# Performance work log

Hardware: AMD Instinct MI355X
Metric: run time of the kernel (lower is better)

## Reference

```python
import jax, jax.numpy as jnp
import numpy as np

HEADS, DIM_HEAD, DIM = 12, 64, 768
H = W = 32
N = H * W
B = 4


def _ln(x, g, b, eps=1e-5):
    mu = x.mean(-1, keepdims=True)
    var = ((x - mu) ** 2).mean(-1, keepdims=True)
    return (x - mu) / jnp.sqrt(var + eps) * g + b


def _get_epipolar(k, src_c2w, target_c2w, h=H, w=W):
    # Faithful port of Epipolar_Attention.get_epipolar, without the (hw*hw,3) repeat
    # materialization (uses broadcasting for the pairwise cross product instead).
    b = k.shape[0]
    Wf = h * 16.0 / 9.0
    k = k.astype(jnp.float32)
    k = k.at[:, 0, :].multiply(Wf).at[:, 1, :].multiply(float(h))
    k = k.at[:, 0, 2].set(h / 2.0).at[:, 1, 2].set(h / 2.0)
    ii, jj = jnp.meshgrid(jnp.arange(h), jnp.arange(w), indexing='ij')
    # after the torch column swap: (col, row, 1)
    coords = jnp.stack([jj.ravel(), ii.ravel(), jnp.ones(h * w, jnp.int32)], axis=1).astype(jnp.float32)  # [hw,3]
    k3 = k[:, :3, :3]
    src_r, src_t = src_c2w[:, :3, :3].astype(jnp.float32), src_c2w[:, :3, 3].astype(jnp.float32)
    tgt_r, tgt_t = target_c2w[:, :3, :3].astype(jnp.float32), target_c2w[:, :3, 3].astype(jnp.float32)
    tgt_rinv = jnp.linalg.inv(tgt_r)
    fx, fy = k3[:, 0, 0][:, None], k3[:, 1, 1][:, None]
    cx, cy = k3[:, 0, 2][:, None], k3[:, 1, 2][:, None]
    nc = jnp.stack([(coords[None, :, 0] - cx) / fx,
                    (coords[None, :, 1] - cy) / fy,
                    jnp.broadcast_to(coords[None, :, 2], (b, h * w))], axis=-1)  # [b,hw,3]
    p3w = jnp.einsum('bij,bnj->bni', src_r, nc) + src_t[:, None]
    p2 = jnp.einsum('bij,bnj->bni', tgt_rinv, p3w) - tgt_t[:, None]  # target_w2c_t = -target_c2w_t
    pij_un = jnp.einsum('bij,bnj->bni', k3, p2)                      # [b,hw,3]
    pij = pij_un / (pij_un[..., -1:] + 1e-6)
    o2 = jnp.einsum('bij,bj->bi', tgt_rinv, src_t) - tgt_t           # origin projected
    oij = jnp.einsum('bij,bj->bi', k3, o2)
    oij = oij / oij[..., -1:]
    oi_to_pi = pij - oij[:, None]                # [b,hw,3]
    oi_to_coord = coords[None] - oij[:, None]    # [b,hw,3]
    cr = jnp.cross(oi_to_pi[:, :, None, :], oi_to_coord[:, None, :, :])  # [b,hw,hw,3]
    area = jnp.sqrt((cr * cr).sum(-1))
    vlen = jnp.sqrt((oi_to_pi * oi_to_pi).sum(-1))[:, :, None]
    dist = area / vlen
    dw = 1.0 - jax.nn.sigmoid(50.0 * (dist - 0.5))
    row_max = dw.max(-1, keepdims=True)
    return jnp.where(row_max < 0.5, 1.0, dw)     # rows with max<0.5 are set to all-ones


def setup_inputs():
    key = jax.random.key(0)
    ks = jax.random.split(key, 16)
    s = 0.02
    x = jax.random.normal(ks[0], (B, N, DIM), jnp.float32)
    src_encode = jax.random.normal(ks[1], (B, N, DIM), jnp.float32)
    intrinsic = (jnp.zeros((B, 4, 4), jnp.float32)
                 .at[:, 0, 0].set(1.0).at[:, 1, 1].set(1.0)
                 .at[:, 0, 2].set(0.5).at[:, 1, 2].set(0.5)
                 .at[:, 2, 2].set(1.0).at[:, 3, 3].set(1.0))
    R = jnp.eye(3, dtype=jnp.float32) + 0.1 * jax.random.normal(ks[2], (2, B, 3, 3), jnp.float32)
    t = 0.5 * jax.random.normal(ks[3], (2, B, 3), jnp.float32)
    c2w = (jnp.zeros((2, B, 4, 4), jnp.float32)
           .at[:, :, :3, :3].set(R).at[:, :, :3, 3].set(t).at[:, :, 3, 3].set(1.0))
    hd = HEADS * DIM_HEAD
    w_ = lambda k_, shp: s * jax.random.normal(k_, shp, jnp.float32)
    return dict(
        x=x, src_encode=src_encode, intrinsic=intrinsic, c2w=c2w,
        lnq_g=jnp.ones(DIM), lnq_b=jnp.zeros(DIM), Wq=w_(ks[4], (DIM, hd)), bq=jnp.zeros(hd),
        lnk_g=jnp.ones(DIM), lnk_b=jnp.zeros(DIM), Wk=w_(ks[5], (DIM, hd)), bk=jnp.zeros(hd),
        lnv_g=jnp.ones(DIM), lnv_b=jnp.zeros(DIM), Wv=w_(ks[6], (DIM, hd)), bv=jnp.zeros(hd),
        Wp=w_(ks[7], (hd, DIM)), bp=jnp.zeros(DIM),
        pre_g=jnp.ones(DIM), pre_b=jnp.zeros(DIM),
        W1=w_(ks[8], (DIM, 2 * DIM)), b1=jnp.zeros(2 * DIM),
        W2=w_(ks[9], (2 * DIM, DIM)), b2=jnp.zeros(DIM),
        post_g=jnp.ones(DIM), post_b=jnp.zeros(DIM))


def reference(x, src_encode, intrinsic, c2w, lnq_g, lnq_b, Wq, bq, lnk_g, lnk_b, Wk, bk,
              lnv_g, lnv_b, Wv, bv, Wp, bp, pre_g, pre_b, W1, b1, W2, b2, post_g, post_b):
    b, n, _ = x.shape
    scale = DIM_HEAD ** -0.5
    split = lambda t_: t_.reshape(b, n, HEADS, DIM_HEAD).transpose(0, 2, 1, 3)  # [b,m,n,d]
    q = split(_ln(x, lnq_g, lnq_b) @ Wq + bq)
    k = split(_ln(src_encode, lnk_g, lnk_b) @ Wk + bk)
    v = split(_ln(src_encode, lnv_g, lnv_b) @ Wv + bv)
    scores = scale * jnp.einsum('bmqd,bmkd->bmqk', q, k)
    e1 = _get_epipolar(intrinsic, c2w[1], c2w[0])                    # do_epipolar
    e2 = jnp.swapaxes(_get_epipolar(intrinsic, c2w[0], c2w[1]), 1, 2)  # bidirectional (transposed)
    wmap = e1 * e2                                                   # [b,n,n], shared across heads
    att = jax.nn.softmax(scores * wmap[:, None], axis=-1)
    a = jnp.einsum('bmqk,bmkd->bmqd', att, v).transpose(0, 2, 1, 3).reshape(b, n, HEADS * DIM_HEAD)
    z = _ln(a @ Wp + bp, pre_g, pre_b)
    z = z + (jax.nn.gelu(z @ W1 + b1, approximate=False) @ W2 + b2)  # torch nn.GELU = exact erf
    z = _ln(z, post_g, post_b)
    wm_full = jnp.broadcast_to(wmap[:, None], (b, HEADS, n, n)).reshape(b * HEADS, n, n)
    return z, wm_full
```

## Files before the change

kernel.cpp:

```cpp
#include <hip/hip_runtime.h>
#include <hip/hip_bf16.h>

typedef unsigned short u16;
typedef __attribute__((ext_vector_type(4))) unsigned short u16x4;
typedef __attribute__((ext_vector_type(8))) unsigned short u16x8;
typedef __attribute__((ext_vector_type(8))) short s16x8;
typedef __attribute__((ext_vector_type(4))) float f32x4;

#define HEADS 12
#define NSEQ 1024
#define DIMM 768
#define DHEAD 64

__device__ __forceinline__ float b2f(u16 h) {
  union { unsigned u; float f; } v; v.u = ((unsigned)h) << 16; return v.f;
}
__device__ __forceinline__ u16 f2b(float f) {
  union { float f; unsigned u; } v; v.f = f;
  unsigned r = v.u + 0x7fffu + ((v.u >> 16) & 1u);
  return (u16)(r >> 16);
}
__device__ __forceinline__ void gl_lds16(const u16* g, u16* l) {
  __builtin_amdgcn_global_load_lds(
      (const __attribute__((address_space(1))) void*)g,
      (__attribute__((address_space(3))) void*)l, 16, 0, 0);
}

template<bool GELU, bool RESID>
__device__ __forceinline__ void gemm_body(
    const u16* __restrict__ A, const u16* __restrict__ BT,
    const float* __restrict__ bias, const u16* __restrict__ resid,
    const float* __restrict__ rg, const float* __restrict__ rb,
    u16* __restrict__ C, int K, int lda, int ldb, int ldc,
    int m0, int n0, u16* As, u16* Bs)
{
  const int tid = threadIdx.x;
  const int lane = tid & 63;
  const int wv = tid >> 6;
  const int wm0 = (wv >> 1) * 64;
  const int wn0 = (wv & 1) * 64;
  const int l15 = lane & 15;
  const int quad = lane >> 4;
  const int srow = lane >> 2;
  const int scol = (lane & 3) * 8;

  f32x4 acc[4][4];
  #pragma unroll
  for (int i = 0; i < 4; ++i)
    #pragma unroll
    for (int j = 0; j < 4; ++j)
      acc[i][j] = {0.f, 0.f, 0.f, 0.f};

  const u16* Ab = A + (long)(m0 + wv * 32 + srow) * lda + scol;
  const u16* Bb = BT + (long)(n0 + wv * 32 + srow) * ldb + scol;
  u16* AsW = As + (wv * 32) * 32;
  u16* BsW = Bs + (wv * 32) * 32;

  auto issue = [&](int buf, int kk) {
    #pragma unroll
    for (int t = 0; t < 2; ++t) {
      gl_lds16(Ab + kk + (long)t * 16 * lda, AsW + buf * 4096 + t * 16 * 32);
      gl_lds16(Bb + kk + (long)t * 16 * ldb, BsW + buf * 4096 + t * 16 * 32);
    }
  };

  const int NK = K >> 5;
  issue(0, 0);
  issue(1, 32);

  int cur = 0;
  for (int i = 0; i < NK; ++i) {
    if (i + 1 < NK) asm volatile("s_waitcnt vmcnt(4)" ::: "memory");
    else            asm volatile("s_waitcnt vmcnt(0)" ::: "memory");
    __builtin_amdgcn_s_barrier();
    __builtin_amdgcn_sched_barrier(0);
    if (i + 2 < NK) {
      int nb = cur + 2; if (nb >= 3) nb -= 3;
      issue(nb, (i + 2) * 32);
    }
    const u16* Ac = As + cur * 4096;
    const u16* Bc = Bs + cur * 4096;
    s16x8 af[4], bfr[4];
    #pragma unroll
    for (int i2 = 0; i2 < 4; ++i2)
      af[i2] = *(const s16x8*)&Ac[(wm0 + i2 * 16 + l15) * 32 + quad * 8];
    #pragma unroll
    for (int j = 0; j < 4; ++j)
      bfr[j] = *(const s16x8*)&Bc[(wn0 + j * 16 + l15) * 32 + quad * 8];
    #pragma unroll
    for (int i2 = 0; i2 < 4; ++i2)
      #pragma unroll
      for (int j = 0; j < 4; ++j)
        acc[i2][j] = __builtin_amdgcn_mfma_f32_16x16x32_bf16(af[i2], bfr[j], acc[i2][j], 0, 0, 0);
    ++cur; if (cur == 3) cur = 0;
  }

  #pragma unroll
  for (int i = 0; i < 4; ++i)
    #pragma unroll
    for (int j = 0; j < 4; ++j) {
      const int col = n0 + wn0 + j * 16 + l15;
      const float bvv = bias[col];
      #pragma unroll
      for (int v = 0; v < 4; ++v) {
        const int row = m0 + wm0 + i * 16 + quad * 4 + v;
        float val = acc[i][j][v] + bvv;
        if (GELU) val = 0.5f * val * (1.0f + erff(val * 0.70710678118654752440f));
        if (RESID) val += b2f(resid[(long)row * ldc + col]) * rg[col] + rb[col];
        C[(long)row * ldc + col] = f2b(val);
      }
    }
}

template<bool GELU, bool RESID>
__device__ __forceinline__ void gemm_body64(
    const u16* __restrict__ A, const u16* __restrict__ BT,
    const float* __restrict__ bias, const u16* __restrict__ resid,
    const float* __restrict__ rg, const float* __restrict__ rb,
    u16* __restrict__ C, int K, int lda, int ldb, int ldc,
    int m0, int n0, u16* As, u16* Bs)
{
  const int tid = threadIdx.x;
  const int lane = tid & 63;
  const int wv = tid >> 6;
  const int wm0 = wv * 32;
  const int l15 = lane & 15;
  const int quad = lane >> 4;
  const int srow = lane >> 2;
  const int scol = (lane & 3) * 8;

  f32x4 acc[2][4];
  #pragma unroll
  for (int i = 0; i < 2; ++i)
    #pragma unroll
    for (int j = 0; j < 4; ++j)
      acc[i][j] = {0.f, 0.f, 0.f, 0.f};

  const u16* Ab = A + (long)(m0 + wv * 32 + srow) * lda + scol;
  const u16* Bb = BT + (long)(n0 + wv * 16 + srow) * ldb + scol;
  u16* AsW = As + (wv * 32) * 32;
  u16* BsW = Bs + (wv * 16) * 32;

  auto issue = [&](int buf, int kk) {
    #pragma unroll
    for (int t = 0; t < 2; ++t)
      gl_lds16(Ab + kk + (long)t * 16 * lda, AsW + buf * 4096 + t * 16 * 32);
    gl_lds16(Bb + kk, BsW + buf * 2048);
  };

  const int NK = K >> 5;
  issue(0, 0);
  issue(1, 32);

  int cur = 0;
  for (int i = 0; i < NK; ++i) {
    if (i + 1 < NK) asm volatile("s_waitcnt vmcnt(3)" ::: "memory");
    else            asm volatile("s_waitcnt vmcnt(0)" ::: "memory");
    __builtin_amdgcn_s_barrier();
    __builtin_amdgcn_sched_barrier(0);
    if (i + 2 < NK) {
      int nb = cur + 2; if (nb >= 3) nb -= 3;
      issue(nb, (i + 2) * 32);
    }
    const u16* Ac = As + cur * 4096;
    const u16* Bc = Bs + cur * 2048;
    s16x8 af[2], bfr[4];
    #pragma unroll
    for (int i2 = 0; i2 < 2; ++i2)
      af[i2] = *(const s16x8*)&Ac[(wm0 + i2 * 16 + l15) * 32 + quad * 8];
    #pragma unroll
    for (int j = 0; j < 4; ++j)
      bfr[j] = *(const s16x8*)&Bc[(j * 16 + l15) * 32 + quad * 8];
    #pragma unroll
    for (int i2 = 0; i2 < 2; ++i2)
      #pragma unroll
      for (int j = 0; j < 4; ++j)
        acc[i2][j] = __builtin_amdgcn_mfma_f32_16x16x32_bf16(af[i2], bfr[j], acc[i2][j], 0, 0, 0);
    ++cur; if (cur == 3) cur = 0;
  }

  #pragma unroll
  for (int i = 0; i < 2; ++i)
    #pragma unroll
    for (int j = 0; j < 4; ++j) {
      const int col = n0 + j * 16 + l15;
      const float bvv = bias[col];
      #pragma unroll
      for (int v = 0; v < 4; ++v) {
        const int row = m0 + wm0 + i * 16 + quad * 4 + v;
        float val = acc[i][j][v] + bvv;
        if (GELU) val = 0.5f * val * (1.0f + erff(val * 0.70710678118654752440f));
        if (RESID) val += b2f(resid[(long)row * ldc + col]) * rg[col] + rb[col];
        C[(long)row * ldc + col] = f2b(val);
      }
    }
}

template<bool GELU, bool RESID>
__global__ __launch_bounds__(256)
void gemm_one(const u16* __restrict__ A, const u16* __restrict__ BT,
              const float* __restrict__ bias, const u16* __restrict__ resid,
              const float* __restrict__ rg, const float* __restrict__ rb,
              u16* __restrict__ C, int K, int lda, int ldb, int ldc)
{
  __shared__ u16 As[12288], Bs[6144];
  gemm_body64<GELU, RESID>(A, BT, bias, resid, rg, rb, C, K, lda, ldb, ldc,
                           blockIdx.x * 128, blockIdx.y * 64, As, Bs);
}

__global__ __launch_bounds__(256)
void gemm_qkv(const u16* __restrict__ nx, const u16* __restrict__ ns,
              const u16* __restrict__ qT, const u16* __restrict__ kvT,
              const float* __restrict__ bqf, const float* __restrict__ bkvf,
              u16* __restrict__ qb, u16* __restrict__ kvb)
{
  __shared__ u16 As[12288], Bs[12288];
  const int z = blockIdx.z;
  if (z == 0)
    gemm_body<false, false>(nx, qT, bqf, nullptr, nullptr, nullptr, qb,
                            768, 768, 768, 768,
                            blockIdx.x * 128, blockIdx.y * 128, As, Bs);
  else
    gemm_body<false, false>(ns, kvT, bkvf, nullptr, nullptr, nullptr, kvb,
                            768, 768, 768, 1536,
                            blockIdx.x * 128, (z - 1) * 768 + blockIdx.y * 128, As, Bs);
}

__global__ __launch_bounds__(256, 3)
void fattn(const u16* __restrict__ qb, const u16* __restrict__ kvb,
           const u16* __restrict__ vT, const u16* __restrict__ wm,
           u16* __restrict__ outA)
{
  __shared__ u16 Qs[2 * 64 * 32];
  __shared__ u16 Ks[2][2 * 64 * 32];
  __shared__ u16 Vs[2][2 * 64 * 32];
  __shared__ u16 Ps[64][72];

  const int bh = blockIdx.y;
  const int b = bh / HEADS, h = bh - b * HEADS;
  const int q0 = blockIdx.x * 64;
  const int tid = threadIdx.x;
  const int lane = tid & 63;
  const int wv = tid >> 6;
  const int l15 = lane & 15;
  const int quad = lane >> 4;
  const int srow = lane >> 2;
  const int scol = (lane & 3) * 8;

  const u16* Qg = qb + ((long)b * NSEQ + q0) * DIMM + h * DHEAD;
  const u16* Kg = kvb + (long)b * NSEQ * 1536 + h * DHEAD;
  const u16* Vg = vT + (long)bh * DHEAD * NSEQ;
  const u16* Wg = wm + ((long)b * NSEQ + q0) * NSEQ;

  #pragma unroll
  for (int h2 = 0; h2 < 2; ++h2) {
    gl_lds16(Qg + (long)(wv * 16 + srow) * DIMM + h2 * 32 + scol,
             Qs + (h2 * 64 + wv * 16) * 32);
    gl_lds16(Kg + (long)(wv * 16 + srow) * 1536 + h2 * 32 + scol,
             Ks[0] + (h2 * 64 + wv * 16) * 32);
    gl_lds16(Vg + (long)(wv * 16 + srow) * NSEQ + h2 * 32 + scol,
             Vs[0] + (h2 * 64 + wv * 16) * 32);
  }

  f32x4 Sacc[4], Oacc[4];
  float mrow[4], lrow[4];
  #pragma unroll
  for (int j = 0; j < 4; ++j) {
    Oacc[j] = {0.f, 0.f, 0.f, 0.f};
    mrow[j] = -3.0e38f;
    lrow[j] = 0.f;
  }
  s16x8 qf[2];

  int cur = 0;
  for (int kt = 0; kt < 16; ++kt) {
    __syncthreads();
    if (kt < 15) {
      const int nxt = cur ^ 1;
      #pragma unroll
      for (int h2 = 0; h2 < 2; ++h2) {
        gl_lds16(Kg + (long)((kt + 1) * 64 + wv * 16 + srow) * 1536 + h2 * 32 + scol,
                 Ks[nxt] + (h2 * 64 + wv * 16) * 32);
        gl_lds16(Vg + (long)(wv * 16 + srow) * NSEQ + (kt + 1) * 64 + h2 * 32 + scol,
                 Vs[nxt] + (h2 * 64 + wv * 16) * 32);
      }
    }

    if (kt == 0) {
      qf[0] = *(const s16x8*)&Qs[(0 * 64 + wv * 16 + l15) * 32 + quad * 8];
      qf[1] = *(const s16x8*)&Qs[(1 * 64 + wv * 16 + l15) * 32 + quad * 8];
    }

    float wr[4][4];
    #pragma unroll
    for (int j = 0; j < 4; ++j)
      #pragma unroll
      for (int v = 0; v < 4; ++v)
        wr[j][v] = b2f(Wg[(long)(wv * 16 + quad * 4 + v) * NSEQ + kt * 64 + j * 16 + l15]);

    #pragma unroll
    for (int j = 0; j < 4; ++j) Sacc[j] = {0.f, 0.f, 0.f, 0.f};
    #pragma unroll
    for (int j = 0; j < 4; ++j)
      #pragma unroll
      for (int h2 = 0; h2 < 2; ++h2) {
        s16x8 kf = *(const s16x8*)&Ks[cur][(h2 * 64 + j * 16 + l15) * 32 + quad * 8];
        Sacc[j] = __builtin_amdgcn_mfma_f32_16x16x32_bf16(qf[h2], kf, Sacc[j], 0, 0, 0);
      }

    #pragma unroll
    for (int j = 0; j < 4; ++j)
      #pragma unroll
      for (int v = 0; v < 4; ++v)
        Sacc[j][v] *= wr[j][v];
    #pragma unroll
    for (int v = 0; v < 4; ++v) {
      float tm = fmaxf(fmaxf(Sacc[0][v], Sacc[1][v]), fmaxf(Sacc[2][v], Sacc[3][v]));
      tm = fmaxf(tm, __shfl_xor(tm, 1));
      tm = fmaxf(tm, __shfl_xor(tm, 2));
      tm = fmaxf(tm, __shfl_xor(tm, 4));
      tm = fmaxf(tm, __shfl_xor(tm, 8));
      const float mnew = fmaxf(mrow[v], tm);
      const float al = __expf(mrow[v] - mnew);
      float rs = 0.f;
      #pragma unroll
      for (int j = 0; j < 4; ++j) {
        const float e = __expf(Sacc[j][v] - mnew);
        Sacc[j][v] = e;
        rs += e;
      }
      rs += __shfl_xor(rs, 1);
      rs += __shfl_xor(rs, 2);
      rs += __shfl_xor(rs, 4);
      rs += __shfl_xor(rs, 8);
      lrow[v] = lrow[v] * al + rs;
      mrow[v] = mnew;
      #pragma unroll
      for (int jn = 0; jn < 4; ++jn) Oacc[jn][v] *= al;
    }
    #pragma unroll
    for (int j = 0; j < 4; ++j)
      #pragma unroll
      for (int v = 0; v < 4; ++v)
        Ps[wv * 16 + quad * 4 + v][j * 16 + l15] = f2b(Sacc[j][v]);

    #pragma unroll
    for (int h2 = 0; h2 < 2; ++h2) {
      s16x8 af = *(const s16x8*)&Ps[wv * 16 + l15][h2 * 32 + quad * 8];
      #pragma unroll
      for (int jn = 0; jn < 4; ++jn) {
        s16x8 vf = *(const s16x8*)&Vs[cur][(h2 * 64 + jn * 16 + l15) * 32 + quad * 8];
        Oacc[jn] = __builtin_amdgcn_mfma_f32_16x16x32_bf16(af, vf, Oacc[jn], 0, 0, 0);
      }
    }
    cur ^= 1;
  }

  #pragma unroll
  for (int v = 0; v < 4; ++v) {
    const int row = q0 + wv * 16 + quad * 4 + v;
    const float inv = 1.0f / lrow[v];
    #pragma unroll
    for (int jn = 0; jn < 4; ++jn)
      outA[((long)(b * NSEQ + row)) * DIMM + h * DHEAD + jn * 16 + l15] =
          f2b(Oacc[jn][v] * inv);
  }
}

template<bool F32IN>
__global__ __launch_bounds__(256)
void norm_k(const void* __restrict__ in, u16* __restrict__ out)
{
  const long base = (long)blockIdx.x * DIMM;
  const int tid = threadIdx.x;
  __shared__ float s1[8], s2[8];
  float v0, v1, v2;
  if (F32IN) {
    const float* p = (const float*)in + base;
    v0 = p[tid]; v1 = p[tid + 256]; v2 = p[tid + 512];
  } else {
    const u16* p = (const u16*)in + base;
    v0 = b2f(p[tid]); v1 = b2f(p[tid + 256]); v2 = b2f(p[tid + 512]);
  }
  float s = v0 + v1 + v2;
  #pragma unroll
  for (int off = 32; off; off >>= 1) s += __shfl_down(s, off);
  const int lane = tid & 63, wid = tid >> 6;
  if (!lane) s1[wid] = s;
  __syncthreads();
  if (!tid) s1[4] = s1[0] + s1[1] + s1[2] + s1[3];
  __syncthreads();
  const float mu = s1[4] / 768.0f;
  float d0 = v0 - mu, d1 = v1 - mu, d2 = v2 - mu;
  float sq = d0 * d0 + d1 * d1 + d2 * d2;
  #pragma unroll
  for (int off = 32; off; off >>= 1) sq += __shfl_down(sq, off);
  if (!lane) s2[wid] = sq;
  __syncthreads();
  if (!tid) s2[4] = s2[0] + s2[1] + s2[2] + s2[3];
  __syncthreads();
  const float rstd = 1.0f / sqrtf(s2[4] / 768.0f + 1e-5f);
  u16* o = out + base;
  o[tid]       = f2b(d0 * rstd);
  o[tid + 256] = f2b(d1 * rstd);
  o[tid + 512] = f2b(d2 * rstd);
}

__global__ __launch_bounds__(256)
void norm_dual(const float* __restrict__ inA, const float* __restrict__ inB,
               u16* __restrict__ outA, u16* __restrict__ outB)
{
  const int r = blockIdx.x;
  const float* p = ((r < 4096) ? inA : inB) + (long)(r & 4095) * DIMM;
  u16* o = ((r < 4096) ? outA : outB) + (long)(r & 4095) * DIMM;
  const int tid = threadIdx.x;
  __shared__ float s1[8], s2[8];
  float v0 = p[tid], v1 = p[tid + 256], v2 = p[tid + 512];
  float s = v0 + v1 + v2;
  #pragma unroll
  for (int off = 32; off; off >>= 1) s += __shfl_down(s, off);
  const int lane = tid & 63, wid = tid >> 6;
  if (!lane) s1[wid] = s;
  __syncthreads();
  if (!tid) s1[4] = s1[0] + s1[1] + s1[2] + s1[3];
  __syncthreads();
  const float mu = s1[4] / 768.0f;
  float d0 = v0 - mu, d1 = v1 - mu, d2 = v2 - mu;
  float sq = d0 * d0 + d1 * d1 + d2 * d2;
  #pragma unroll
  for (int off = 32; off; off >>= 1) sq += __shfl_down(sq, off);
  if (!lane) s2[wid] = sq;
  __syncthreads();
  if (!tid) s2[4] = s2[0] + s2[1] + s2[2] + s2[3];
  __syncthreads();
  const float rstd = 1.0f / sqrtf(s2[4] / 768.0f + 1e-5f);
  o[tid]       = f2b(d0 * rstd);
  o[tid + 256] = f2b(d1 * rstd);
  o[tid + 512] = f2b(d2 * rstd);
}

__global__ __launch_bounds__(256)
void ln_final(const u16* __restrict__ in, const float* __restrict__ g,
              const float* __restrict__ bb, float* __restrict__ out)
{
  const long base = (long)blockIdx.x * DIMM;
  const int tid = threadIdx.x;
  __shared__ float s1[8], s2[8];
  const u16* p = in + base;
  float v0 = b2f(p[tid]), v1 = b2f(p[tid + 256]), v2 = b2f(p[tid + 512]);
  float s = v0 + v1 + v2;
  #pragma unroll
  for (int off = 32; off; off >>= 1) s += __shfl_down(s, off);
  const int lane = tid & 63, wid = tid >> 6;
  if (!lane) s1[wid] = s;
  __syncthreads();
  if (!tid) s1[4] = s1[0] + s1[1] + s1[2] + s1[3];
  __syncthreads();
  const float mu = s1[4] / 768.0f;
  float d0 = v0 - mu, d1 = v1 - mu, d2 = v2 - mu;
  float sq = d0 * d0 + d1 * d1 + d2 * d2;
  #pragma unroll
  for (int off = 32; off; off >>= 1) sq += __shfl_down(sq, off);
  if (!lane) s2[wid] = sq;
  __syncthreads();
  if (!tid) s2[4] = s2[0] + s2[1] + s2[2] + s2[3];
  __syncthreads();
  const float rstd = 1.0f / sqrtf(s2[4] / 768.0f + 1e-5f);
  float* o = out + base;
  o[tid]       = d0 * rstd * g[tid]       + bb[tid];
  o[tid + 256] = d1 * rstd * g[tid + 256] + bb[tid + 256];
  o[tid + 512] = d2 * rstd * g[tid + 512] + bb[tid + 512];
}

__global__ __launch_bounds__(256)
void prep_all(const float* w0, const float* w1, const float* w2,
              const float* w3, const float* w4, const float* w5,
              const float* gq, const float* gk, const float* gv, const float* gp,
              u16* d0, u16* d12, u16* d3, u16* d4, u16* d5,
              const float* bq, const float* bk, const float* bv, const float* b1,
              const float* lnqb, const float* lnkb, const float* lnvb, const float* preb,
              float* obq, float* obkv, float* ob1)
{
  __shared__ u16 t[32][36];
  __shared__ float red[8][32];
  const int tid = threadIdx.x;

  if (blockIdx.z == 6) {
    const int y = blockIdx.y;
    if (y >= 4) return;
    const float* W; const float* bln; const float* bw; float* out;
    int C; float sc = 1.0f;
    switch (y) {
      case 0: W = w0; bln = lnqb; bw = bq; out = obq;        C = 768;  sc = 0.125f; break;
      case 1: W = w1; bln = lnkb; bw = bk; out = obkv;       C = 768;  break;
      case 2: W = w2; bln = lnvb; bw = bv; out = obkv + 768; C = 768;  break;
      default: W = w4; bln = preb; bw = b1; out = ob1;       C = 1536; break;
    }
    const int c0 = blockIdx.x * 32;
    if (c0 >= C) return;
    const int cl = tid & 31;
    const int rg = tid >> 5;
    const int c = c0 + cl;
    float s = 0.f;
    for (int r = rg * 96; r < rg * 96 + 96; ++r)
      s += bln[r] * W[(long)r * C + c];
    red[rg][cl] = s;
    __syncthreads();
    if (rg == 0) {
      float tot = bw[c];
      #pragma unroll
      for (int k = 0; k < 8; ++k) tot += red[k][cl];
      out[c] = tot * sc;
    }
    return;
  }

  const float* src; const float* g; u16* dst; int R, C; float sc = 1.0f;
  switch (blockIdx.z) {
    case 0: src = w0; g = gq; dst = d0;  R = 768;  C = 768;  sc = 0.125f; break;
    case 1: src = w1; g = gk; dst = d12; R = 768;  C = 768;  break;
    case 2: src = w2; g = gv; dst = d12 + 768 * 768; R = 768; C = 768; break;
    case 3: src = w3; g = nullptr; dst = d3; R = 768;  C = 768;  break;
    case 4: src = w4; g = gp; dst = d4; R = 768;  C = 1536; break;
    default: src = w5; g = nullptr; dst = d5; R = 1536; C = 768; break;
  }
  const int c0 = blockIdx.x * 32;
  const int r0 = blockIdx.y * 32;
  if (c0 >= C || r0 >= R) return;
  const int i = tid >> 3;
  const int j4 = (tid & 7) * 4;
  const float rs = (g ? g[r0 + i] : 1.0f) * sc;
  #pragma unroll
  for (int jj = 0; jj < 4; ++jj)
    t[i][j4 + jj] = f2b(src[(long)(r0 + i) * C + c0 + j4 + jj] * rs);
  __syncthreads();
  u16x4 ov;
  #pragma unroll
  for (int jj = 0; jj < 4; ++jj) ov[jj] = t[j4 + jj][i];
  *(u16x4*)&dst[(long)(c0 + i) * R + r0 + j4] = ov;
}

__global__ __launch_bounds__(256)
void v_transpose(const u16* __restrict__ kvb, u16* __restrict__ vT)
{
  __shared__ u16 t[64][72];
  const int z = blockIdx.y;
  const int b = z / HEADS, h = z - b * HEADS;
  const int n0 = blockIdx.x * 64;
  const int tid = threadIdx.x;
  const int i = tid >> 2;
  const int jb = (tid & 3) * 16;
  const u16* src = kvb + (long)(b * NSEQ + n0 + i) * 1536 + 768 + h * DHEAD + jb;
  *(u16x8*)&t[i][jb]     = *(const u16x8*)&src[0];
  *(u16x8*)&t[i][jb + 8] = *(const u16x8*)&src[8];
  __syncthreads();
  const int dd = tid >> 2;
  const int nb = (tid & 3) * 16;
  u16x8 o0, o1;
  #pragma unroll
  for (int nn = 0; nn < 8; ++nn) { o0[nn] = t[nb + nn][dd]; o1[nn] = t[nb + 8 + nn][dd]; }
  u16* dst = vT + ((long)z * DHEAD + dd) * NSEQ + n0 + nb;
  *(u16x8*)&dst[0] = o0;
  *(u16x8*)&dst[8] = o1;
}

__global__ void epi_setup(const float* __restrict__ intr, const float* __restrict__ c2w,
                          float* __restrict__ u4, float* __restrict__ oijb)
{
  const int db = blockIdx.x;
  const int d = db >> 2, b = db & 3;
  __shared__ float S[36];
  if (threadIdx.x == 0) {
    const int sidx = (d == 0) ? 1 : 0;
    const int tidx = 1 - sidx;
    float k3[9], sr[9], st[3], tr[9], tt[3];
    const float Wf = 32.0f * 16.0f / 9.0f;
    for (int j = 0; j < 3; ++j) {
      k3[j]     = intr[(b * 4 + 0) * 4 + j] * Wf;
      k3[3 + j] = intr[(b * 4 + 1) * 4 + j] * 32.0f;
      k3[6 + j] = intr[(b * 4 + 2) * 4 + j];
    }
    k3[2] = 16.0f; k3[5] = 16.0f;
    for (int i = 0; i < 3; ++i) {
      for (int j = 0; j < 3; ++j) {
        sr[i * 3 + j] = c2w[((sidx * 4 + b) * 4 + i) * 4 + j];
        tr[i * 3 + j] = c2w[((tidx * 4 + b) * 4 + i) * 4 + j];
      }
      st[i] = c2w[((sidx * 4 + b) * 4 + i) * 4 + 3];
      tt[i] = c2w[((tidx * 4 + b) * 4 + i) * 4 + 3];
    }
    double a = tr[0], bb_ = tr[1], c = tr[2];
    double dd2 = tr[3], e = tr[4], f = tr[5];
    double g2 = tr[6], h2 = tr[7], i2 = tr[8];
    double det = a * (e * i2 - f * h2) - bb_ * (dd2 * i2 - f * g2) + c * (dd2 * h2 - e * g2);
    double inv[9] = {
      (e * i2 - f * h2), (c * h2 - bb_ * i2), (bb_ * f - c * e),
      (f * g2 - dd2 * i2), (a * i2 - c * g2), (c * dd2 - a * f),
      (dd2 * h2 - e * g2), (bb_ * g2 - a * h2), (a * e - bb_ * dd2)
    };
    float tri[9];
    for (int t2 = 0; t2 < 9; ++t2) tri[t2] = (float)(inv[t2] / det);
    float o2[3], oij[3];
    for (int i3 = 0; i3 < 3; ++i3)
      o2[i3] = tri[i3 * 3] * st[0] + tri[i3 * 3 + 1] * st[1] + tri[i3 * 3 + 2] * st[2] - tt[i3];
    for (int i3 = 0; i3 < 3; ++i3)
      oij[i3] = k3[i3 * 3] * o2[0] + k3[i3 * 3 + 1] * o2[1] + k3[i3 * 3 + 2] * o2[2];
    const float ozf = oij[2];
    oij[0] = oij[0] / ozf; oij[1] = oij[1] / ozf; oij[2] = ozf / ozf;
    for (int t2 = 0; t2 < 9; ++t2) { S[t2] = k3[t2]; S[9 + t2] = sr[t2]; S[21 + t2] = tri[t2]; }
    for (int t2 = 0; t2 < 3; ++t2) { S[18 + t2] = st[t2]; S[30 + t2] = tt[t2]; S[33 + t2] = oij[t2]; }
    oijb[db * 4 + 0] = oij[0]; oijb[db * 4 + 1] = oij[1]; oijb[db * 4 + 2] = oij[2];
    oijb[db * 4 + 3] = 0.f;
  }
  __syncthreads();
  for (int n = threadIdx.x; n < 1024; n += blockDim.x) {
    const float ncx = ((float)(n & 31) - S[2]) / S[0];
    const float ncy = ((float)(n >> 5) - S[5]) / S[4];
    const float p0 = S[9]  * ncx + S[10] * ncy + S[11] + S[18];
    const float p1 = S[12] * ncx + S[13] * ncy + S[14] + S[19];
    const float p2 = S[15] * ncx + S[16] * ncy + S[17] + S[20];
    const float q0 = S[21] * p0 + S[22] * p1 + S[23] * p2 - S[30];
    const float q1 = S[24] * p0 + S[25] * p1 + S[26] * p2 - S[31];
    const float q2 = S[27] * p0 + S[28] * p1 + S[29] * p2 - S[32];
    const float w0 = S[0] * q0 + S[1] * q1 + S[2] * q2;
    const float w1 = S[3] * q0 + S[4] * q1 + S[5] * q2;
    const float w2 = S[6] * q0 + S[7] * q1 + S[8] * q2;
    const float pz = w2 + 1e-6f;
    const float ux = w0 / pz - S[33];
    const float uy = w1 / pz - S[34];
    const float uz = w2 / pz - S[35];
    const float vlen = sqrtf(ux * ux + uy * uy + uz * uz);
    f32x4 uo = {ux, uy, uz, vlen};
    *(f32x4*)&u4[((long)db * 1024 + n) * 4] = uo;
  }
}

__device__ __forceinline__ float dwval(f32x4 U, float ox, float oy, float oz, int m)
{
  const float cx = (float)(m & 31) - ox;
  const float cy = (float)(m >> 5) - oy;
  const float cz = 1.0f - oz;
  const float crx = U.y * cz - U.z * cy;
  const float cry = U.z * cx - U.x * cz;
  const float crz = U.x * cy - U.y * cx;
  const float area = sqrtf(crx * crx + cry * cry + crz * crz);
  const float dist = area / U.w;
  const float t = 50.0f * (dist - 0.5f);
  return 1.0f - 1.0f / (1.0f + __expf(-t));
}

__global__ __launch_bounds__(256)
void epi_flags(const float* __restrict__ u4, const float* __restrict__ oijb,
               float* __restrict__ flags)
{
  const int rowid = blockIdx.x;
  const int db = rowid >> 10;
  const f32x4 U = *(const f32x4*)&u4[(long)rowid * 4];
  const float ox = oijb[db * 4 + 0];
  const float oy = oijb[db * 4 + 1];
  const float oz = oijb[db * 4 + 2];
  const int tid = threadIdx.x;
  __shared__ float red[8];
  float mx = -1e30f;
  #pragma unroll
  for (int i = 0; i < 4; ++i)
    mx = fmaxf(mx, dwval(U, ox, oy, oz, tid + i * 256));
  #pragma unroll
  for (int off = 32; off; off >>= 1) mx = fmaxf(mx, __shfl_down(mx, off));
  const int lane = tid & 63, wid = tid >> 6;
  if (!lane) red[wid] = mx;
  __syncthreads();
  if (!tid) {
    const float m4 = fmaxf(fmaxf(red[0], red[1]), fmaxf(red[2], red[3]));
    flags[rowid] = (m4 < 0.5f) ? 1.0f : 0.0f;
  }
}

__global__ __launch_bounds__(256)
void epi_wmap(const float* __restrict__ u4, const float* __restrict__ oijb,
              const float* __restrict__ flags,
              u16* __restrict__ wm, float* __restrict__ wm_full)
{
  const int b = blockIdx.z;
  const int q0 = blockIdx.x * 32;
  const int k0 = blockIdx.y * 32;
  const int tid = threadIdx.x;
  const int i = tid >> 3;
  const int j4 = (tid & 7) * 4;

  __shared__ f32x4 U2s[32];
  __shared__ float f2s[32];
  __shared__ float f1s[32];
  if (tid < 32) {
    U2s[tid] = *(const f32x4*)&u4[((long)(4 + b) * 1024 + k0 + tid) * 4];
    f2s[tid] = flags[(4 + b) * 1024 + k0 + tid];
    f1s[tid] = flags[b * 1024 + q0 + tid];
  }
  __syncthreads();

  const int q = q0 + i;
  const f32x4 U1 = *(const f32x4*)&u4[((long)b * 1024 + q) * 4];
  const float o1x = oijb[b * 4 + 0], o1y = oijb[b * 4 + 1], o1z = oijb[b * 4 + 2];
  const float o2x = oijb[(4 + b) * 4 + 0], o2y = oijb[(4 + b) * 4 + 1], o2z = oijb[(4 + b) * 4 + 2];
  const bool fl1 = f1s[i] > 0.5f;

  u16x4 pk;
  f32x4 wf;
  #pragma unroll
  for (int jj = 0; jj < 4; ++jj) {
    const int k = k0 + j4 + jj;
    const float e1 = fl1 ? 1.0f : dwval(U1, o1x, o1y, o1z, k);
    const float e2 = (f2s[j4 + jj] > 0.5f) ? 1.0f : dwval(U2s[j4 + jj], o2x, o2y, o2z, q);
    const float w = e1 * e2;
    wf[jj] = w;
    pk[jj] = f2b(w);
  }
  *(u16x4*)&wm[((long)b * 1024 + q0 + i) * 1024 + k0 + j4] = pk;
  #pragma unroll
  for (int h = 0; h < HEADS; ++h)
    *(f32x4*)&wm_full[((long)(b * HEADS + h) * 1024 + q0 + i) * 1024 + k0 + j4] = wf;
}

extern "C" void kernel_launch(void* const* d_in, const int* in_sizes, int n_in,
                              void* d_out, int out_size, void* d_ws, size_t ws_size,
                              hipStream_t stream)
{
  (void)in_sizes; (void)n_in; (void)out_size; (void)ws_size;
  const float* x     = (const float*)d_in[0];
  const float* src   = (const float*)d_in[1];
  const float* intr  = (const float*)d_in[2];
  const float* c2w   = (const float*)d_in[3];
  const float* lnq_g = (const float*)d_in[4];
  const float* lnq_b = (const float*)d_in[5];
  const float* Wq    = (const float*)d_in[6];
  const float* bq    = (const float*)d_in[7];
  const float* lnk_g = (const float*)d_in[8];
  const float* lnk_b = (const float*)d_in[9];
  const float* Wk    = (const float*)d_in[10];
  const float* bk    = (const float*)d_in[11];
  const float* lnv_g = (const float*)d_in[12];
  const float* lnv_b = (const float*)d_in[13];
  const float* Wv    = (const float*)d_in[14];
  const float* bv    = (const float*)d_in[15];
  const float* Wp    = (const float*)d_in[16];
  const float* bp    = (const float*)d_in[17];
  const float* pre_g = (const float*)d_in[18];
  const float* pre_b = (const float*)d_in[19];
  const float* W1    = (const float*)d_in[20];
  const float* b1    = (const float*)d_in[21];
  const float* W2    = (const float*)d_in[22];
  const float* b2    = (const float*)d_in[23];
  const float* post_g= (const float*)d_in[24];
  const float* post_b= (const float*)d_in[25];

  char* ws = (char*)d_ws;
  size_t off = 0;
  auto alloc = [&](size_t bytes) -> char* {
    char* p = ws + off;
    off = (off + bytes + 255) & ~(size_t)255;
    return p;
  };
  const size_t SEQD = (size_t)4096 * 768 * 2;

  u16* WqT  = (u16*)alloc(768 * 768 * 2);
  u16* WkvT = (u16*)alloc((size_t)1536 * 768 * 2);
  u16* WpT  = (u16*)alloc(768 * 768 * 2);
  u16* W1T  = (u16*)alloc(768 * 1536 * 2);
  u16* W2T  = (u16*)alloc(1536 * 768 * 2);
  float* bqf  = (float*)alloc(768 * 4);
  float* bkvf = (float*)alloc(1536 * 4);
  float* b1f  = (float*)alloc(1536 * 4);
  char* pool = alloc(6 * SEQD);
  float* u4   = (float*)alloc(8 * 1024 * 4 * 4);
  float* oijb = (float*)alloc(8 * 4 * 4);
  u16* wmapb  = (u16*)alloc((size_t)4 * 1024 * 1024 * 2);
  float* flagb = (float*)alloc(8 * 1024 * 4);

  u16* S0 = (u16*)pool;
  u16* S1 = (u16*)(pool + SEQD);
  u16* S2 = (u16*)(pool + 2 * SEQD);
  u16* S3 = (u16*)(pool + 3 * SEQD);
  u16* S5 = (u16*)(pool + 5 * SEQD);

  float* out_z  = (float*)d_out;
  float* out_wm = (float*)d_out + (size_t)4 * 1024 * 768;

  prep_all<<<dim3(48, 48, 7), 256, 0, stream>>>(
      Wq, Wk, Wv, Wp, W1, W2, lnq_g, lnk_g, lnv_g, pre_g,
      WqT, WkvT, WpT, W1T, W2T,
      bq, bk, bv, b1, lnq_b, lnk_b, lnv_b, pre_b,
      bqf, bkvf, b1f);

  epi_setup<<<8, 128, 0, stream>>>(intr, c2w, u4, oijb);
  epi_flags<<<8192, 256, 0, stream>>>(u4, oijb, flagb);
  epi_wmap<<<dim3(32, 32, 4), 256, 0, stream>>>(u4, oijb, flagb, wmapb, out_wm);

  norm_dual<<<8192, 256, 0, stream>>>(x, src, S0, S1);

  gemm_qkv<<<dim3(32, 6, 3), 256, 0, stream>>>(S0, S1, WqT, WkvT, bqf, bkvf, S2, S3);

  v_transpose<<<dim3(16, 48), 256, 0, stream>>>(S3, S5);

  fattn<<<dim3(16, 48), 256, 0, stream>>>(S2, S3, S5, wmapb, S0);

  gemm_one<false, false><<<dim3(32, 12), 256, 0, stream>>>(
      S0, WpT, bp, nullptr, nullptr, nullptr, S1, 768, 768, 768, 768);

  norm_k<false><<<4096, 256, 0, stream>>>(S1, S2);

  gemm_one<true, false><<<dim3(32, 24), 256, 0, stream>>>(
      S2, W1T, b1f, nullptr, nullptr, nullptr, S3, 768, 768, 768, 1536);

  gemm_one<false, true><<<dim3(32, 12), 256, 0, stream>>>(
      S3, W2T, b2, S2, pre_g, pre_b, S5, 1536, 1536, 1536, 768);

  ln_final<<<4096, 256, 0, stream>>>(S5, post_g, post_b, out_z);
}
```

Before: 511.5 us.

## Fuse launches: merge prep with input norm, QKV GEMM with epipolar map and V-transpose

Folds the input LayerNorm into the weight-prep kernel as extra blocks. It also builds a combined stageB kernel that runs the QKV GEMM blocks alongside the epipolar weight-map blocks. The V projection is now written transposed straight from the GEMM epilogue through LDS, so the separate v_transpose pass is gone. The aim is fewer launches and less serialisation between small, independent stages. The cost is a staged epilogue with extra barriers and mixed block types sharing one grid.

```diff
diff --git a/kernel.cpp b/kernel.cpp
--- a/kernel.cpp
+++ b/kernel.cpp
@@ -26,13 +26,13 @@
       (__attribute__((address_space(3))) void*)l, 16, 0, 0);
 }
 
-template<bool GELU, bool RESID>
+template<bool GELU, bool RESID, bool VTOUT>
 __device__ __forceinline__ void gemm_body(
     const u16* __restrict__ A, const u16* __restrict__ BT,
     const float* __restrict__ bias, const u16* __restrict__ resid,
     const float* __restrict__ rg, const float* __restrict__ rb,
     u16* __restrict__ C, int K, int lda, int ldb, int ldc,
-    int m0, int n0, u16* As, u16* Bs)
+    int m0, int n0, u16* As, u16* Bs, u16* __restrict__ vt)
 {
   const int tid = threadIdx.x;
   const int lane = tid & 63;
@@ -95,6 +95,40 @@
     ++cur; if (cur == 3) cur = 0;
   }
 
+  if (VTOUT) {
+    __syncthreads();
+    u16* shp = As;
+    const int b = m0 >> 10;
+    const int nloc = m0 & 1023;
+    const int fb0 = n0 - 768;
+    #pragma unroll
+    for (int p = 0; p < 2; ++p) {
+      if ((wv & 1) == p) {
+        #pragma unroll
+        for (int j = 0; j < 4; ++j) {
+          const float bvv = bias[n0 + wn0 + j * 16 + l15];
+          #pragma unroll
+          for (int i = 0; i < 4; ++i)
+            #pragma unroll
+            for (int v = 0; v < 4; ++v)
+              shp[(j * 16 + l15) * 136 + (wm0 + i * 16 + quad * 4 + v)] =
+                  f2b(acc[i][j][v] + bvv);
+        }
+      }
+      __syncthreads();
+      {
+        const int f = tid >> 2;
+        const int rg2 = (tid & 3) * 32;
+        u16* dst = vt + ((long)(b * 768 + fb0 + p * 64 + f)) * NSEQ + nloc + rg2;
+        #pragma unroll
+        for (int c4 = 0; c4 < 4; ++c4)
+          *(u16x8*)&dst[c4 * 8] = *(const u16x8*)&shp[f * 136 + rg2 + c4 * 8];
+      }
+      __syncthreads();
+    }
+    return;
+  }
+
   #pragma unroll
   for (int i = 0; i < 4; ++i)
     #pragma unroll
@@ -208,286 +242,73 @@
                            blockIdx.x * 128, blockIdx.y * 64, As, Bs);
 }
 
+__device__ __forceinline__ float dwval(f32x4 U, float ox, float oy, float oz, int m)
+{
+  const float cx = (float)(m & 31) - ox;
+  const float cy = (float)(m >> 5) - oy;
+  const float cz = 1.0f - oz;
+  const float crx = U.y * cz - U.z * cy;
+  const float cry = U.z * cx - U.x * cz;
+  const float crz = U.x * cy - U.y * cx;
+  const float area = sqrtf(crx * crx + cry * cry + crz * crz);
+  const float dist = area / U.w;
+  const float t = 50.0f * (dist - 0.5f);
+  return 1.0f - 1.0f / (1.0f + __expf(-t));
+}
+
+#define PREP_T0 13824
+#define PREP_T1 14016
+#define PREP_T2 22208
+
 __global__ __launch_bounds__(256)
-void gemm_qkv(const u16* __restrict__ nx, const u16* __restrict__ ns,
-              const u16* __restrict__ qT, const u16* __restrict__ kvT,
-              const float* __restrict__ bqf, const float* __restrict__ bkvf,
-              u16* __restrict__ qb, u16* __restrict__ kvb)
-{
-  __shared__ u16 As[12288], Bs[12288];
-  const int z = blockIdx.z;
-  if (z == 0)
-    gemm_body<false, false>(nx, qT, bqf, nullptr, nullptr, nullptr, qb,
-                            768, 768, 768, 768,
-                            blockIdx.x * 128, blockIdx.y * 128, As, Bs);
-  else
-    gemm_body<false, false>(ns, kvT, bkvf, nullptr, nullptr, nullptr, kvb,
-                            768, 768, 768, 1536,
-                            blockIdx.x * 128, (z - 1) * 768 + blockIdx.y * 128, As, Bs);
-}
-
-__global__ __launch_bounds__(256, 3)
-void fattn(const u16* __restrict__ qb, const u16* __restrict__ kvb,
-           const u16* __restrict__ vT, const u16* __restrict__ wm,
-           u16* __restrict__ outA)
-{
-  __shared__ u16 Qs[2 * 64 * 32];
-  __shared__ u16 Ks[2][2 * 64 * 32];
-  __shared__ u16 Vs[2][2 * 64 * 32];
-  __shared__ u16 Ps[64][72];
-
-  const int bh = blockIdx.y;
-  const int b = bh / HEADS, h = bh - b * HEADS;
-  const int q0 = blockIdx.x * 64;
+void prep2(const float* w0, const float* w1, const float* w2,
+           const float* w3, const float* w4, const float* w5,
+           const float* gq, const float* gk, const float* gv, const float* gp,
+           u16* d0, u16* d12, u16* d3, u16* d4, u16* d5,
+           const float* bq, const float* bk, const float* bv, const float* b1,
+           const float* lnqb, const float* lnkb, const float* lnvb, const float* preb,
+           float* obq, float* obkv, float* ob1,
+           const float* nx, const float* nsrc, u16* onx, u16* onsrc)
+{
+  const int bid = blockIdx.x;
   const int tid = threadIdx.x;
-  const int lane = tid & 63;
-  const int wv = tid >> 6;
-  const int l15 = lane & 15;
-  const int quad = lane >> 4;
-  const int srow = lane >> 2;
-  const int scol = (lane & 3) * 8;
-
-  const u16* Qg = qb + ((long)b * NSEQ + q0) * DIMM + h * DHEAD;
-  const u16* Kg = kvb + (long)b * NSEQ * 1536 + h * DHEAD;
-  const u16* Vg = vT + (long)bh * DHEAD * NSEQ;
-  const u16* Wg = wm + ((long)b * NSEQ + q0) * NSEQ;
-
-  #pragma unroll
-  for (int h2 = 0; h2 < 2; ++h2) {
-    gl_lds16(Qg + (long)(wv * 16 + srow) * DIMM + h2 * 32 + scol,
-             Qs + (h2 * 64 + wv * 16) * 32);
-    gl_lds16(Kg + (long)(wv * 16 + srow) * 1536 + h2 * 32 + scol,
-             Ks[0] + (h2 * 64 + wv * 16) * 32);
-    gl_lds16(Vg + (long)(wv * 16 + srow) * NSEQ + h2 * 32 + scol,
-             Vs[0] + (h2 * 64 + wv * 16) * 32);
-  }
-
-  f32x4 Sacc[4], Oacc[4];
-  float mrow[4], lrow[4];
-  #pragma unroll
-  for (int j = 0; j < 4; ++j) {
-    Oacc[j] = {0.f, 0.f, 0.f, 0.f};
-    mrow[j] = -3.0e38f;
-    lrow[j] = 0.f;
-  }
-  s16x8 qf[2];
-
-  int cur = 0;
-  for (int kt = 0; kt < 16; ++kt) {
+
+  if (bid < PREP_T0) {
+    __shared__ u16 t[32][36];
+    const int z = bid / 2304;
+    const int rem = bid - z * 2304;
+    const int bx = rem % 48, by = rem / 48;
+    const float* src; const float* g; u16* dst; int R, C; float sc = 1.0f;
+    switch (z) {
+      case 0: src = w0; g = gq; dst = d0;  R = 768;  C = 768;  sc = 0.125f; break;
+      case 1: src = w1; g = gk; dst = d12; R = 768;  C = 768;  break;
+      case 2: src = w2; g = gv; dst = d12 + 768 * 768; R = 768; C = 768; break;
+      case 3: src = w3; g = nullptr; dst = d3; R = 768;  C = 768;  break;
+      case 4: src = w4; g = gp; dst = d4; R = 768;  C = 1536; break;
+      default: src = w5; g = nullptr; dst = d5; R = 1536; C = 768; break;
+    }
+    const int c0 = bx * 32;
+    const int r0 = by * 32;
+    if (c0 >= C || r0 >= R) return;
+    const int i = tid >> 3;
+    const int j4 = (tid & 7) * 4;
+    const float rs = (g ? g[r0 + i] : 1.0f) * sc;
+    #pragma unroll
+    for (int jj = 0; jj < 4; ++jj)
+      t[i][j4 + jj] = f2b(src[(long)(r0 + i) * C + c0 + j4 + jj] * rs);
     __syncthreads();
-    if (kt < 15) {
-      const int nxt = cur ^ 1;
-      #pragma unroll
-      for (int h2 = 0; h2 < 2; ++h2) {
-        gl_lds16(Kg + (long)((kt + 1) * 64 + wv * 16 + srow) * 1536 + h2 * 32 + scol,
-                 Ks[nxt] + (h2 * 64 + wv * 16) * 32);
-        gl_lds16(Vg + (long)(wv * 16 + srow) * NSEQ + (kt + 1) * 64 + h2 * 32 + scol,
-                 Vs[nxt] + (h2 * 64 + wv * 16) * 32);
-      }
-    }
-
-    if (kt == 0) {
-      qf[0] = *(const s16x8*)&Qs[(0 * 64 + wv * 16 + l15) * 32 + quad * 8];
-      qf[1] = *(const s16x8*)&Qs[(1 * 64 + wv * 16 + l15) * 32 + quad * 8];
-    }
-
-    float wr[4][4];
-    #pragma unroll
-    for (int j = 0; j < 4; ++j)
-      #pragma unroll
-      for (int v = 0; v < 4; ++v)
-        wr[j][v] = b2f(Wg[(long)(wv * 16 + quad * 4 + v) * NSEQ + kt * 64 + j * 16 + l15]);
-
-    #pragma unroll
-    for (int j = 0; j < 4; ++j) Sacc[j] = {0.f, 0.f, 0.f, 0.f};
-    #pragma unroll
-    for (int j = 0; j < 4; ++j)
-      #pragma unroll
-      for (int h2 = 0; h2 < 2; ++h2) {
-        s16x8 kf = *(const s16x8*)&Ks[cur][(h2 * 64 + j * 16 + l15) * 32 + quad * 8];
-        Sacc[j] = __builtin_amdgcn_mfma_f32_16x16x32_bf16(qf[h2], kf, Sacc[j], 0, 0, 0);
-      }
-
-    #pragma unroll
-    for (int j = 0; j < 4; ++j)
-      #pragma unroll
-      for (int v = 0; v < 4; ++v)
-        Sacc[j][v] *= wr[j][v];
-    #pragma unroll
-    for (int v = 0; v < 4; ++v) {
-      float tm = fmaxf(fmaxf(Sacc[0][v], Sacc[1][v]), fmaxf(Sacc[2][v], Sacc[3][v]));
-      tm = fmaxf(tm, __shfl_xor(tm, 1));
-      tm = fmaxf(tm, __shfl_xor(tm, 2));
-      tm = fmaxf(tm, __shfl_xor(tm, 4));
-      tm = fmaxf(tm, __shfl_xor(tm, 8));
-      const float mnew = fmaxf(mrow[v], tm);
-      const float al = __expf(mrow[v] - mnew);
-      float rs = 0.f;
-      #pragma unroll
-      for (int j = 0; j < 4; ++j) {
-        const float e = __expf(Sacc[j][v] - mnew);
-        Sacc[j][v] = e;
-        rs += e;
-      }
-      rs += __shfl_xor(rs, 1);
-      rs += __shfl_xor(rs, 2);
-      rs += __shfl_xor(rs, 4);
-      rs += __shfl_xor(rs, 8);
-      lrow[v] = lrow[v] * al + rs;
-      mrow[v] = mnew;
-      #pragma unroll
-      for (int jn = 0; jn < 4; ++jn) Oacc[jn][v] *= al;
-    }
-    #pragma unroll
-    for (int j = 0; j < 4; ++j)
-      #pragma unroll
-      for (int v = 0; v < 4; ++v)
-        Ps[wv * 16 + quad * 4 + v][j * 16 + l15] = f2b(Sacc[j][v]);
-
-    #pragma unroll
-    for (int h2 = 0; h2 < 2; ++h2) {
-      s16x8 af = *(const s16x8*)&Ps[wv * 16 + l15][h2 * 32 + quad * 8];
-      #pragma unroll
-      for (int jn = 0; jn < 4; ++jn) {
-        s16x8 vf = *(const s16x8*)&Vs[cur][(h2 * 64 + jn * 16 + l15) * 32 + quad * 8];
-        Oacc[jn] = __builtin_amdgcn_mfma_f32_16x16x32_bf16(af, vf, Oacc[jn], 0, 0, 0);
-      }
-    }
-    cur ^= 1;
-  }
-
-  #pragma unroll
-  for (int v = 0; v < 4; ++v) {
-    const int row = q0 + wv * 16 + quad * 4 + v;
-    const float inv = 1.0f / lrow[v];
-    #pragma unroll
-    for (int jn = 0; jn < 4; ++jn)
-      outA[((long)(b * NSEQ + row)) * DIMM + h * DHEAD + jn * 16 + l15] =
-          f2b(Oacc[jn][v] * inv);
-  }
-}
-
-template<bool F32IN>
-__global__ __launch_bounds__(256)
-void norm_k(const void* __restrict__ in, u16* __restrict__ out)
-{
-  const long base = (long)blockIdx.x * DIMM;
-  const int tid = threadIdx.x;
-  __shared__ float s1[8], s2[8];
-  float v0, v1, v2;
-  if (F32IN) {
-    const float* p = (const float*)in + base;
-    v0 = p[tid]; v1 = p[tid + 256]; v2 = p[tid + 512];
-  } else {
-    const u16* p = (const u16*)in + base;
-    v0 = b2f(p[tid]); v1 = b2f(p[tid + 256]); v2 = b2f(p[tid + 512]);
-  }
-  float s = v0 + v1 + v2;
-  #pragma unroll
-  for (int off = 32; off; off >>= 1) s += __shfl_down(s, off);
-  const int lane = tid & 63, wid = tid >> 6;
-  if (!lane) s1[wid] = s;
-  __syncthreads();
-  if (!tid) s1[4] = s1[0] + s1[1] + s1[2] + s1[3];
-  __syncthreads();
-  const float mu = s1[4] / 768.0f;
-  float d0 = v0 - mu, d1 = v1 - mu, d2 = v2 - mu;
-  float sq = d0 * d0 + d1 * d1 + d2 * d2;
-  #pragma unroll
-  for (int off = 32; off; off >>= 1) sq += __shfl_down(sq, off);
-  if (!lane) s2[wid] = sq;
-  __syncthreads();
-  if (!tid) s2[4] = s2[0] + s2[1] + s2[2] + s2[3];
-  __syncthreads();
-  const float rstd = 1.0f / sqrtf(s2[4] / 768.0f + 1e-5f);
-  u16* o = out + base;
-  o[tid]       = f2b(d0 * rstd);
-  o[tid + 256] = f2b(d1 * rstd);
-  o[tid + 512] = f2b(d2 * rstd);
-}
-
-__global__ __launch_bounds__(256)
-void norm_dual(const float* __restrict__ inA, const float* __restrict__ inB,
-               u16* __restrict__ outA, u16* __restrict__ outB)
-{
-  const int r = blockIdx.x;
-  const float* p = ((r < 4096) ? inA : inB) + (long)(r & 4095) * DIMM;
-  u16* o = ((r < 4096) ? outA : outB) + (long)(r & 4095) * DIMM;
-  const int tid = threadIdx.x;
-  __shared__ float s1[8], s2[8];
-  float v0 = p[tid], v1 = p[tid + 256], v2 = p[tid + 512];
-  float s = v0 + v1 + v2;
-  #pragma unroll
-  for (int off = 32; off; off >>= 1) s += __shfl_down(s, off);
-  const int lane = tid & 63, wid = tid >> 6;
-  if (!lane) s1[wid] = s;
-  __syncthreads();
-  if (!tid) s1[4] = s1[0] + s1[1] + s1[2] + s1[3];
-  __syncthreads();
-  const float mu = s1[4] / 768.0f;
-  float d0 = v0 - mu, d1 = v1 - mu, d2 = v2 - mu;
-  float sq = d0 * d0 + d1 * d1 + d2 * d2;
-  #pragma unroll
-  for (int off = 32; off; off >>= 1) sq += __shfl_down(sq, off);
-  if (!lane) s2[wid] = sq;
-  __syncthreads();
-  if (!tid) s2[4] = s2[0] + s2[1] + s2[2] + s2[3];
-  __syncthreads();
-  const float rstd = 1.0f / sqrtf(s2[4] / 768.0f + 1e-5f);
-  o[tid]       = f2b(d0 * rstd);
-  o[tid + 256] = f2b(d1 * rstd);
-  o[tid + 512] = f2b(d2 * rstd);
-}
-
-__global__ __launch_bounds__(256)
-void ln_final(const u16* __restrict__ in, const float* __restrict__ g,
-              const float* __restrict__ bb, float* __restrict__ out)
-{
-  const long base = (long)blockIdx.x * DIMM;
-  const int tid = threadIdx.x;
-  __shared__ float s1[8], s2[8];
-  const u16* p = in + base;
-  float v0 = b2f(p[tid]), v1 = b2f(p[tid + 256]), v2 = b2f(p[tid + 512]);
-  float s = v0 + v1 + v2;
-  #pragma unroll
-  for (int off = 32; off; off >>= 1) s += __shfl_down(s, off);
-  const int lane = tid & 63, wid = tid >> 6;
-  if (!lane) s1[wid] = s;
-  __syncthreads();
-  if (!tid) s1[4] = s1[0] + s1[1] + s1[2] + s1[3];
-  __syncthreads();
-  const float mu = s1[4] / 768.0f;
-  float d0 = v0 - mu, d1 = v1 - mu, d2 = v2 - mu;
-  float sq = d0 * d0 + d1 * d1 + d2 * d2;
-  #pragma unroll
-  for (int off = 32; off; off >>= 1) sq += __shfl_down(sq, off);
-  if (!lane) s2[wid] = sq;
-  __syncthreads();
-  if (!tid) s2[4] = s2[0] + s2[1] + s2[2] + s2[3];
-  __syncthreads();
-  const float rstd = 1.0f / sqrtf(s2[4] / 768.0f + 1e-5f);
-  float* o = out + base;
-  o[tid]       = d0 * rstd * g[tid]       + bb[tid];
-  o[tid + 256] = d1 * rstd * g[tid + 256] + bb[tid + 256];
-  o[tid + 512] = d2 * rstd * g[tid + 512] + bb[tid + 512];
-}
-
-__global__ __launch_bounds__(256)
-void prep_all(const float* w0, const float* w1, const float* w2,
-              const float* w3, const float* w4, const float* w5,
-              const float* gq, const float* gk, const float* gv, const float* gp,
-              u16* d0, u16* d12, u16* d3, u16* d4, u16* d5,
-              const float* bq, const float* bk, const float* bv, const float* b1,
-              const float* lnqb, const float* lnkb, const float* lnvb, const float* preb,
-              float* obq, float* obkv, float* ob1)
-{
-  __shared__ u16 t[32][36];
-  __shared__ float red[8][32];
-  const int tid = threadIdx.x;
-
-  if (blockIdx.z == 6) {
-    const int y = blockIdx.y;
-    if (y >= 4) return;
+    u16x4 ov;
+    #pragma unroll
+    for (int jj = 0; jj < 4; ++jj) ov[jj] = t[j4 + jj][i];
+    *(u16x4*)&dst[(long)(c0 + i) * R + r0 + j4] = ov;
+    return;
+  }
+
+  if (bid < PREP_T1) {
+    __shared__ float red[8][32];
+    const int idx = bid - PREP_T0;
+    const int y = idx / 48;
+    const int bx = idx % 48;
     const float* W; const float* bln; const float* bw; float* out;
     int C; float sc = 1.0f;
     switch (y) {
@@ -496,7 +317,7 @@
       case 2: W = w2; bln = lnvb; bw = bv; out = obkv + 768; C = 768;  break;
       default: W = w4; bln = preb; bw = b1; out = ob1;       C = 1536; break;
     }
-    const int c0 = blockIdx.x * 32;
+    const int c0 = bx * 32;
     if (c0 >= C) return;
     const int cl = tid & 31;
     const int rg = tid >> 5;
@@ -515,53 +336,34 @@
     return;
   }
 
-  const float* src; const float* g; u16* dst; int R, C; float sc = 1.0f;
-  switch (blockIdx.z) {
-    case 0: src = w0; g = gq; dst = d0;  R = 768;  C = 768;  sc = 0.125f; break;
-    case 1: src = w1; g = gk; dst = d12; R = 768;  C = 768;  break;
-    case 2: src = w2; g = gv; dst = d12 + 768 * 768; R = 768; C = 768; break;
-    case 3: src = w3; g = nullptr; dst = d3; R = 768;  C = 768;  break;
-    case 4: src = w4; g = gp; dst = d4; R = 768;  C = 1536; break;
-    default: src = w5; g = nullptr; dst = d5; R = 1536; C = 768; break;
-  }
-  const int c0 = blockIdx.x * 32;
-  const int r0 = blockIdx.y * 32;
-  if (c0 >= C || r0 >= R) return;
-  const int i = tid >> 3;
-  const int j4 = (tid & 7) * 4;
-  const float rs = (g ? g[r0 + i] : 1.0f) * sc;
-  #pragma unroll
-  for (int jj = 0; jj < 4; ++jj)
-    t[i][j4 + jj] = f2b(src[(long)(r0 + i) * C + c0 + j4 + jj] * rs);
-  __syncthreads();
-  u16x4 ov;
-  #pragma unroll
-  for (int jj = 0; jj < 4; ++jj) ov[jj] = t[j4 + jj][i];
-  *(u16x4*)&dst[(long)(c0 + i) * R + r0 + j4] = ov;
-}
-
-__global__ __launch_bounds__(256)
-void v_transpose(const u16* __restrict__ kvb, u16* __restrict__ vT)
-{
-  __shared__ u16 t[64][72];
-  const int z = blockIdx.y;
-  const int b = z / HEADS, h = z - b * HEADS;
-  const int n0 = blockIdx.x * 64;
-  const int tid = threadIdx.x;
-  const int i = tid >> 2;
-  const int jb = (tid & 3) * 16;
-  const u16* src = kvb + (long)(b * NSEQ + n0 + i) * 1536 + 768 + h * DHEAD + jb;
-  *(u16x8*)&t[i][jb]     = *(const u16x8*)&src[0];
-  *(u16x8*)&t[i][jb + 8] = *(const u16x8*)&src[8];
-  __syncthreads();
-  const int dd = tid >> 2;
-  const int nb = (tid & 3) * 16;
-  u16x8 o0, o1;
-  #pragma unroll
-  for (int nn = 0; nn < 8; ++nn) { o0[nn] = t[nb + nn][dd]; o1[nn] = t[nb + 8 + nn][dd]; }
-  u16* dst = vT + ((long)z * DHEAD + dd) * NSEQ + n0 + nb;
-  *(u16x8*)&dst[0] = o0;
-  *(u16x8*)&dst[8] = o1;
+  {
+    __shared__ float s1[8], s2[8];
+    const int r = bid - PREP_T1;
+    const float* p = ((r < 4096) ? nx : nsrc) + (long)(r & 4095) * DIMM;
+    u16* o = ((r < 4096) ? onx : onsrc) + (long)(r & 4095) * DIMM;
+    float v0 = p[tid], v1 = p[tid + 256], v2 = p[tid + 512];
+    float s = v0 + v1 + v2;
+    #pragma unroll
+    for (int off = 32; off; off >>= 1) s += __shfl_down(s, off);
+    const int lane = tid & 63, wid = tid >> 6;
+    if (!lane) s1[wid] = s;
+    __syncthreads();
+    if (!tid) s1[4] = s1[0] + s1[1] + s1[2] + s1[3];
+    __syncthreads();
+    const float mu = s1[4] / 768.0f;
+    float d0 = v0 - mu, d1 = v1 - mu, d2 = v2 - mu;
+    float sq = d0 * d0 + d1 * d1 + d2 * d2;
+    #pragma unroll
+    for (int off = 32; off; off >>= 1) sq += __shfl_down(sq, off);
+    if (!lane) s2[wid] = sq;
+    __syncthreads();
+    if (!tid) s2[4] = s2[0] + s2[1] + s2[2] + s2[3];
+    __syncthreads();
+    const float rstd = 1.0f / sqrtf(s2[4] / 768.0f + 1e-5f);
+    o[tid]       = f2b(d0 * rstd);
+    o[tid + 256] = f2b(d1 * rstd);
+    o[tid + 512] = f2b(d2 * rstd);
+  }
 }
 
 __global__ void epi_setup(const float* __restrict__ intr, const float* __restrict__ c2w,
@@ -635,20 +437,6 @@
   }
 }
 
-__device__ __forceinline__ float dwval(f32x4 U, float ox, float oy, float oz, int m)
-{
-  const float cx = (float)(m & 31) - ox;
-  const float cy = (float)(m >> 5) - oy;
-  const float cz = 1.0f - oz;
-  const float crx = U.y * cz - U.z * cy;
-  const float cry = U.z * cx - U.x * cz;
-  const float crz = U.x * cy - U.y * cx;
-  const float area = sqrtf(crx * crx + cry * cry + crz * crz);
-  const float dist = area / U.w;
-  const float t = 50.0f * (dist - 0.5f);
-  return 1.0f - 1.0f / (1.0f + __expf(-t));
-}
-
 __global__ __launch_bounds__(256)
 void epi_flags(const float* __restrict__ u4, const float* __restrict__ oijb,
                float* __restrict__ flags)
@@ -677,20 +465,52 @@
 }
 
 __global__ __launch_bounds__(256)
-void epi_wmap(const float* __restrict__ u4, const float* __restrict__ oijb,
-              const float* __restrict__ flags,
-              u16* __restrict__ wm, float* __restrict__ wm_full)
-{
-  const int b = blockIdx.z;
-  const int q0 = blockIdx.x * 32;
-  const int k0 = blockIdx.y * 32;
+void stageB(const u16* __restrict__ nx, const u16* __restrict__ ns,
+            const u16* __restrict__ qT, const u16* __restrict__ kvT,
+            const float* __restrict__ bqf, const float* __restrict__ bkvf,
+            u16* __restrict__ qb, u16* __restrict__ kvb, u16* __restrict__ vT,
+            const float* __restrict__ u4, const float* __restrict__ oijb,
+            const float* __restrict__ flags,
+            u16* __restrict__ wm, float* __restrict__ wm_full)
+{
+  __shared__ __align__(16) u16 sh[24576];
+  const int bid = blockIdx.x;
   const int tid = threadIdx.x;
+
+  if (bid < 576) {
+    u16* As = sh;
+    u16* Bs = sh + 12288;
+    const int x = bid & 31;
+    const int t = bid >> 5;
+    const int y = t % 6;
+    const int z = t / 6;
+    if (z == 0)
+      gemm_body<false, false, false>(nx, qT, bqf, nullptr, nullptr, nullptr, qb,
+                                     768, 768, 768, 768,
+                                     x * 128, y * 128, As, Bs, nullptr);
+    else if (z == 1)
+      gemm_body<false, false, false>(ns, kvT, bkvf, nullptr, nullptr, nullptr, kvb,
+                                     768, 768, 768, 1536,
+                                     x * 128, y * 128, As, Bs, nullptr);
+    else
+      gemm_body<false, false, true>(ns, kvT, bkvf, nullptr, nullptr, nullptr, nullptr,
+                                    768, 768, 768, 1536,
+                                    x * 128, 768 + y * 128, As, Bs, vT);
+    return;
+  }
+
+  const int id = bid - 576;
+  const int qx = id & 31;
+  const int ky = (id >> 5) & 31;
+  const int b = id >> 10;
+  const int q0 = qx * 32;
+  const int k0 = ky * 32;
   const int i = tid >> 3;
   const int j4 = (tid & 7) * 4;
 
-  __shared__ f32x4 U2s[32];
-  __shared__ float f2s[32];
-  __shared__ float f1s[32];
+  f32x4* U2s = (f32x4*)sh;
+  float* f2s = (float*)(sh + 256);
+  float* f1s = (float*)(sh + 320);
   if (tid < 32) {
     U2s[tid] = *(const f32x4*)&u4[((long)(4 + b) * 1024 + k0 + tid) * 4];
     f2s[tid] = flags[(4 + b) * 1024 + k0 + tid];
@@ -719,6 +539,212 @@
   #pragma unroll
   for (int h = 0; h < HEADS; ++h)
     *(f32x4*)&wm_full[((long)(b * HEADS + h) * 1024 + q0 + i) * 1024 + k0 + j4] = wf;
+}
+
+__global__ __launch_bounds__(256, 3)
+void fattn(const u16* __restrict__ qb, const u16* __restrict__ kvb,
+           const u16* __restrict__ vT, const u16* __restrict__ wm,
+           u16* __restrict__ outA)
+{
+  __shared__ u16 Qs[2 * 64 * 32];
+  __shared__ u16 Ks[2][2 * 64 * 32];
+  __shared__ u16 Vs[2][2 * 64 * 32];
+  __shared__ u16 Ps[64][72];
+
+  const int bh = blockIdx.y;
+  const int b = bh / HEADS, h = bh - b * HEADS;
+  const int q0 = blockIdx.x * 64;
+  const int tid = threadIdx.x;
+  const int lane = tid & 63;
+  const int wv = tid >> 6;
+  const int l15 = lane & 15;
+  const int quad = lane >> 4;
+  const int srow = lane >> 2;
+  const int scol = (lane & 3) * 8;
+
+  const u16* Qg = qb + ((long)b * NSEQ + q0) * DIMM + h * DHEAD;
+  const u16* Kg = kvb + (long)b * NSEQ * 1536 + h * DHEAD;
+  const u16* Vg = vT + (long)bh * DHEAD * NSEQ;
+  const u16* Wg = wm + ((long)b * NSEQ + q0) * NSEQ;
+
+  #pragma unroll
+  for (int h2 = 0; h2 < 2; ++h2) {
+    gl_lds16(Qg + (long)(wv * 16 + srow) * DIMM + h2 * 32 + scol,
+             Qs + (h2 * 64 + wv * 16) * 32);
+    gl_lds16(Kg + (long)(wv * 16 + srow) * 1536 + h2 * 32 + scol,
+             Ks[0] + (h2 * 64 + wv * 16) * 32);
+    gl_lds16(Vg + (long)(wv * 16 + srow) * NSEQ + h2 * 32 + scol,
+             Vs[0] + (h2 * 64 + wv * 16) * 32);
+  }
+
+  f32x4 Sacc[4], Oacc[4];
+  float mrow[4], lrow[4];
+  #pragma unroll
+  for (int j = 0; j < 4; ++j) {
+    Oacc[j] = {0.f, 0.f, 0.f, 0.f};
+    mrow[j] = -3.0e38f;
+    lrow[j] = 0.f;
+  }
+  s16x8 qf[2];
+
+  int cur = 0;
+  for (int kt = 0; kt < 16; ++kt) {
+    __syncthreads();
+    if (kt < 15) {
+      const int nxt = cur ^ 1;
+      #pragma unroll
+      for (int h2 = 0; h2 < 2; ++h2) {
+        gl_lds16(Kg + (long)((kt + 1) * 64 + wv * 16 + srow) * 1536 + h2 * 32 + scol,
+                 Ks[nxt] + (h2 * 64 + wv * 16) * 32);
+        gl_lds16(Vg + (long)(wv * 16 + srow) * NSEQ + (kt + 1) * 64 + h2 * 32 + scol,
+                 Vs[nxt] + (h2 * 64 + wv * 16) * 32);
+      }
+    }
+
+    if (kt == 0) {
+      qf[0] = *(const s16x8*)&Qs[(0 * 64 + wv * 16 + l15) * 32 + quad * 8];
+      qf[1] = *(const s16x8*)&Qs[(1 * 64 + wv * 16 + l15) * 32 + quad * 8];
+    }
+
+    float wr[4][4];
+    #pragma unroll
+    for (int j = 0; j < 4; ++j)
+      #pragma unroll
+      for (int v = 0; v < 4; ++v)
+        wr[j][v] = b2f(Wg[(long)(wv * 16 + quad * 4 + v) * NSEQ + kt * 64 + j * 16 + l15]);
+
+    #pragma unroll
+    for (int j = 0; j < 4; ++j) Sacc[j] = {0.f, 0.f, 0.f, 0.f};
+    #pragma unroll
+    for (int j = 0; j < 4; ++j)
+      #pragma unroll
+      for (int h2 = 0; h2 < 2; ++h2) {
+        s16x8 kf = *(const s16x8*)&Ks[cur][(h2 * 64 + j * 16 + l15) * 32 + quad * 8];
+        Sacc[j] = __builtin_amdgcn_mfma_f32_16x16x32_bf16(qf[h2], kf, Sacc[j], 0, 0, 0);
+      }
+
+    #pragma unroll
+    for (int j = 0; j < 4; ++j)
+      #pragma unroll
+      for (int v = 0; v < 4; ++v)
+        Sacc[j][v] *= wr[j][v];
+    #pragma unroll
+    for (int v = 0; v < 4; ++v) {
+      float tm = fmaxf(fmaxf(Sacc[0][v], Sacc[1][v]), fmaxf(Sacc[2][v], Sacc[3][v]));
+      tm = fmaxf(tm, __shfl_xor(tm, 1));
+      tm = fmaxf(tm, __shfl_xor(tm, 2));
+      tm = fmaxf(tm, __shfl_xor(tm, 4));
+      tm = fmaxf(tm, __shfl_xor(tm, 8));
+      const float mnew = fmaxf(mrow[v], tm);
+      const float al = __expf(mrow[v] - mnew);
+      float rs = 0.f;
+      #pragma unroll
+      for (int j = 0; j < 4; ++j) {
+        const float e = __expf(Sacc[j][v] - mnew);
+        Sacc[j][v] = e;
+        rs += e;
+      }
+      rs += __shfl_xor(rs, 1);
+      rs += __shfl_xor(rs, 2);
+      rs += __shfl_xor(rs, 4);
+      rs += __shfl_xor(rs, 8);
+      lrow[v] = lrow[v] * al + rs;
+      mrow[v] = mnew;
+      #pragma unroll
+      for (int jn = 0; jn < 4; ++jn) Oacc[jn][v] *= al;
+    }
+    #pragma unroll
+    for (int j = 0; j < 4; ++j)
+      #pragma unroll
+      for (int v = 0; v < 4; ++v)
+        Ps[wv * 16 + quad * 4 + v][j * 16 + l15] = f2b(Sacc[j][v]);
+
+    #pragma unroll
+    for (int h2 = 0; h2 < 2; ++h2) {
+      s16x8 af = *(const s16x8*)&Ps[wv * 16 + l15][h2 * 32 + quad * 8];
+      #pragma unroll
+      for (int jn = 0; jn < 4; ++jn) {
+        s16x8 vf = *(const s16x8*)&Vs[cur][(h2 * 64 + jn * 16 + l15) * 32 + quad * 8];
+        Oacc[jn] = __builtin_amdgcn_mfma_f32_16x16x32_bf16(af, vf, Oacc[jn], 0, 0, 0);
+      }
+    }
+    cur ^= 1;
+  }
+
+  #pragma unroll
+  for (int v = 0; v < 4; ++v) {
+    const int row = q0 + wv * 16 + quad * 4 + v;
+    const float inv = 1.0f / lrow[v];
+    #pragma unroll
+    for (int jn = 0; jn < 4; ++jn)
+      outA[((long)(b * NSEQ + row)) * DIMM + h * DHEAD + jn * 16 + l15] =
+          f2b(Oacc[jn][v] * inv);
+  }
+}
+
+__global__ __launch_bounds__(256)
+void norm_k(const u16* __restrict__ in, u16* __restrict__ out)
+{
+  const long base = (long)blockIdx.x * DIMM;
+  const int tid = threadIdx.x;
+  __shared__ float s1[8], s2[8];
+  const u16* p = in + base;
+  float v0 = b2f(p[tid]), v1 = b2f(p[tid + 256]), v2 = b2f(p[tid + 512]);
+  float s = v0 + v1 + v2;
+  #pragma unroll
+  for (int off = 32; off; off >>= 1) s += __shfl_down(s, off);
+  const int lane = tid & 63, wid = tid >> 6;
+  if (!lane) s1[wid] = s;
+  __syncthreads();
+  if (!tid) s1[4] = s1[0] + s1[1] + s1[2] + s1[3];
+  __syncthreads();
+  const float mu = s1[4] / 768.0f;
+  float d0 = v0 - mu, d1 = v1 - mu, d2 = v2 - mu;
+  float sq = d0 * d0 + d1 * d1 + d2 * d2;
+  #pragma unroll
+  for (int off = 32; off; off >>= 1) sq += __shfl_down(sq, off);
+  if (!lane) s2[wid] = sq;
+  __syncthreads();
+  if (!tid) s2[4] = s2[0] + s2[1] + s2[2] + s2[3];
+  __syncthreads();
+  const float rstd = 1.0f / sqrtf(s2[4] / 768.0f + 1e-5f);
+  u16* o = out + base;
+  o[tid]       = f2b(d0 * rstd);
+  o[tid + 256] = f2b(d1 * rstd);
+  o[tid + 512] = f2b(d2 * rstd);
+}
+
+__global__ __launch_bounds__(256)
+void ln_final(const u16* __restrict__ in, const float* __restrict__ g,
+              const float* __restrict__ bb, float* __restrict__ out)
+{
+  const long base = (long)blockIdx.x * DIMM;
+  const int tid = threadIdx.x;
+  __shared__ float s1[8], s2[8];
+  const u16* p = in + base;
+  float v0 = b2f(p[tid]), v1 = b2f(p[tid + 256]), v2 = b2f(p[tid + 512]);
+  float s = v0 + v1 + v2;
+  #pragma unroll
+  for (int off = 32; off; off >>= 1) s += __shfl_down(s, off);
+  const int lane = tid & 63, wid = tid >> 6;
+  if (!lane) s1[wid] = s;
+  __syncthreads();
+  if (!tid) s1[4] = s1[0] + s1[1] + s1[2] + s1[3];
+  __syncthreads();
+  const float mu = s1[4] / 768.0f;
+  float d0 = v0 - mu, d1 = v1 - mu, d2 = v2 - mu;
+  float sq = d0 * d0 + d1 * d1 + d2 * d2;
+  #pragma unroll
+  for (int off = 32; off; off >>= 1) sq += __shfl_down(sq, off);
+  if (!lane) s2[wid] = sq;
+  __syncthreads();
+  if (!tid) s2[4] = s2[0] + s2[1] + s2[2] + s2[3];
+  __syncthreads();
+  const float rstd = 1.0f / sqrtf(s2[4] / 768.0f + 1e-5f);
+  float* o = out + base;
+  o[tid]       = d0 * rstd * g[tid]       + bb[tid];
+  o[tid + 256] = d1 * rstd * g[tid + 256] + bb[tid + 256];
+  o[tid + 512] = d2 * rstd * g[tid + 512] + bb[tid + 512];
 }
 
 extern "C" void kernel_launch(void* const* d_in, const int* in_sizes, int n_in,
@@ -785,28 +811,26 @@
   float* out_z  = (float*)d_out;
   float* out_wm = (float*)d_out + (size_t)4 * 1024 * 768;
 
-  prep_all<<<dim3(48, 48, 7), 256, 0, stream>>>(
+  prep2<<<PREP_T2, 256, 0, stream>>>(
       Wq, Wk, Wv, Wp, W1, W2, lnq_g, lnk_g, lnv_g, pre_g,
       WqT, WkvT, WpT, W1T, W2T,
       bq, bk, bv, b1, lnq_b, lnk_b, lnv_b, pre_b,
-      bqf, bkvf, b1f);
+      bqf, bkvf, b1f,
+      x, src, S0, S1);
 
   epi_setup<<<8, 128, 0, stream>>>(intr, c2w, u4, oijb);
   epi_flags<<<8192, 256, 0, stream>>>(u4, oijb, flagb);
-  epi_wmap<<<dim3(32, 32, 4), 256, 0, stream>>>(u4, oijb, flagb, wmapb, out_wm);
-
-  norm_dual<<<8192, 256, 0, stream>>>(x, src, S0, S1);
-
-  gemm_qkv<<<dim3(32, 6, 3), 256, 0, stream>>>(S0, S1, WqT, WkvT, bqf, bkvf, S2, S3);
-
-  v_transpose<<<dim3(16, 48), 256, 0, stream>>>(S3, S5);
+
+  stageB<<<4672, 256, 0, stream>>>(
+      S0, S1, WqT, WkvT, bqf, bkvf, S2, S3, S5,
+      u4, oijb, flagb, wmapb, out_wm);
 
   fattn<<<dim3(16, 48), 256, 0, stream>>>(S2, S3, S5, wmapb, S0);
 
   gemm_one<false, false><<<dim3(32, 12), 256, 0, stream>>>(
       S0, WpT, bp, nullptr, nullptr, nullptr, S1, 768, 768, 768, 768);
 
-  norm_k<false><<<4096, 256, 0, stream>>>(S1, S2);
+  norm_k<<<4096, 256, 0, stream>>>(S1, S2);
 
   gemm_one<true, false><<<dim3(32, 24), 256, 0, stream>>>(
       S2, W1T, b1f, nullptr, nullptr, nullptr, S3, 768, 768, 768, 1536);
```

Result: faster. 484.3 us (-5.3%).
